# Performance work log

Hardware: AMD Instinct MI355X
Metric: run time of the kernel (lower is better)

## Reference

```python
import jax, jax.numpy as jnp
import numpy as np

B, D, UD = 32, 1024, 256          # batch, chunks_dim, units_dim
ENT, NENT = 32, 64                # entity_size, n_entities
S, C = NENT * ENT, NENT + 1       # src_len (units), n_chunks
NEG_INF = float('-inf')


def setup_inputs() -> dict:
    key = jax.random.key(0)
    ks = jax.random.split(key, 9)
    source = jax.random.normal(ks[0], (B, D), jnp.float32)
    high_level_repr = jax.random.normal(ks[1], (C, B, D), jnp.float32)
    pos_embs = jax.random.normal(ks[2], (S, B, UD), jnp.float32)
    low_level_repr = jax.random.normal(ks[3], (S, B, D), jnp.float32)
    low_level_mask = jax.random.randint(ks[4], (NENT, B, ENT), 0, 2).astype(bool)
    high_level_mask = jax.random.randint(ks[5], (1, B, C), 0, 2).astype(bool)
    high_level_mask = high_level_mask.at[..., 0].set(False)  # avoid all-masked chunk softmax
    W_unit = jax.random.normal(ks[6], (UD, D), jnp.float32) / np.sqrt(D)
    W_chunk = jax.random.normal(ks[7], (D, D), jnp.float32) / np.sqrt(D)
    W_out = jax.random.normal(ks[8], (D, 2 * D), jnp.float32) / np.sqrt(2 * D)
    return {"source": source, "high_level_repr": high_level_repr, "pos_embs": pos_embs,
            "low_level_repr": low_level_repr, "low_level_mask": low_level_mask,
            "high_level_mask": high_level_mask, "W_unit": W_unit, "W_chunk": W_chunk,
            "W_out": W_out}


def reference(source, high_level_repr, pos_embs, low_level_repr,
              low_level_mask, high_level_mask, W_unit, W_chunk, W_out):
    # batch-first views (torch transposes(0,1))
    hl = jnp.swapaxes(high_level_repr, 0, 1)    # (B, C, D)
    ll = jnp.swapaxes(low_level_repr, 0, 1)     # (B, S, D)
    pe = jnp.swapaxes(pos_embs, 0, 1)           # (B, S, UD)
    ll_mask = jnp.swapaxes(low_level_mask, 0, 1)   # (B, NENT, ENT)
    hl_mask = jnp.swapaxes(high_level_mask, 0, 1)  # (B, 1, C)

    # 'general' attention scorers, tgt_len == 1
    q_u = source @ W_unit.T                      # (B, UD)
    align_units = jnp.einsum('bd,bsd->bs', q_u, pe)        # (B, S)
    q_c = source @ W_chunk.T                     # (B, D)
    align_chunks = jnp.einsum('bd,bcd->bc', q_c, hl)[:, None, :]  # (B, 1, C)

    # low-level masked softmax per entity, NaN rows -> 0
    au = align_units.reshape(B, NENT, ENT)
    au = jnp.where(ll_mask, NEG_INF, au)
    au = jax.nn.softmax(au, axis=-1)
    all_masked = jnp.all(ll_mask, axis=-1)       # (B, NENT) rows that were NaN
    au = jnp.where(all_masked[..., None], 0.0, au)
    au = au.reshape(B, 1, S)

    # high-level masked softmax, drop chunk 0, inflate to unit granularity
    ac = jnp.where(hl_mask, NEG_INF, align_chunks)
    ac = jax.nn.softmax(ac, axis=-1)[:, :, 1:]   # (B, 1, C-1)
    ac_inflated = jnp.repeat(ac, ENT, axis=-1)   # (B, 1, S)

    align_vectors = ac_inflated * au             # (B, 1, S)
    c = jnp.einsum('bts,bsd->btd', align_vectors, ll)  # (B, 1, D)
    concat = jnp.concatenate([c, source[:, None, :]], axis=-1).reshape(B, 2 * D)
    attn_h = jnp.tanh(concat @ W_out.T)          # (B, D); tanh since attn_type='general'

    return (attn_h,
            align_vectors[:, 0, :],              # (B, S)
            ac[:, 0, :],                         # (B, C-1)
            au.reshape(B, S))                    # (B, S)
```

## Files before the change

kernel.cpp:

```cpp
#include <hip/hip_runtime.h>

#define B 32
#define D 1024
#define UD 256
#define ENT 32
#define NENT 64
#define S 2048
#define C 65

__device__ __forceinline__ float dot4(float4 w, const float* q) {
    return w.x * q[0] + w.y * q[1] + w.z * q[2] + w.w * q[3];
}

__global__ __launch_bounds__(256) void k_proj(const float* __restrict__ src,
                                              const float* __restrict__ Wu,
                                              const float* __restrict__ Wc,
                                              float* __restrict__ qu,
                                              float* __restrict__ qc) {
    __shared__ alignas(16) float s_src[4][D];
    __shared__ float red[4][64][4];
    int t = threadIdx.x, rg = blockIdx.x, bg = blockIdx.y;
    for (int f = t; f < 4 * (D / 4); f += 256) {
        int bb = f >> 8, i4 = f & 255;
        float4 v = *(const float4*)(src + (size_t)(bg * 4 + bb) * D + i4 * 4);
        *(float4*)(&s_src[bb][i4 * 4]) = v;
    }
    __syncthreads();
    int jl = t & 63, kq = t >> 6;
    int gj = rg * 64 + jl;
    const float* wrow = (gj < UD) ? (Wu + (size_t)gj * D) : (Wc + (size_t)(gj - UD) * D);
    const float4* wp = (const float4*)wrow + kq * 64;
    float acc[4] = {0.f, 0.f, 0.f, 0.f};
#pragma unroll 4
    for (int i = 0; i < 64; ++i) {
        float4 w = wp[i];
        int k = kq * 256 + i * 4;
#pragma unroll
        for (int bb = 0; bb < 4; ++bb) acc[bb] += dot4(w, &s_src[bb][k]);
    }
#pragma unroll
    for (int bb = 0; bb < 4; ++bb) red[kq][jl][bb] = acc[bb];
    __syncthreads();
    {
        int jl2 = t & 63, bb = t >> 6;
        float s = red[0][jl2][bb] + red[1][jl2][bb] + red[2][jl2][bb] + red[3][jl2][bb];
        int gj2 = rg * 64 + jl2, b = bg * 4 + bb;
        if (gj2 < UD) qu[b * UD + gj2] = s;
        else qc[b * D + (gj2 - UD)] = s;
    }
}

__global__ __launch_bounds__(256) void k_units(const float* __restrict__ pe,
                                               const int* __restrict__ lmask,
                                               const float* __restrict__ qu,
                                               float* __restrict__ out_au) {
    __shared__ alignas(16) float q[UD];
    __shared__ float part[256];
    int n = blockIdx.x, b = blockIdx.y, t = threadIdx.x;
    q[t] = qu[b * UD + t];
    __syncthreads();
    int e = t >> 3, r = t & 7;
    const float4* pp = (const float4*)(pe + (size_t)(n * ENT + e) * B * UD + (size_t)b * UD) + r * 8;
    float acc = 0.f;
#pragma unroll
    for (int i = 0; i < 8; ++i) acc += dot4(pp[i], &q[(r * 8 + i) * 4]);
    part[t] = acc;
    __syncthreads();
    if (t < ENT) {
        float sc = 0.f;
#pragma unroll
        for (int r2 = 0; r2 < 8; ++r2) sc += part[t * 8 + r2];
        bool m = lmask[(size_t)n * B * ENT + b * ENT + t] != 0;
        float v = m ? -1e30f : sc;
        float mx = v;
        for (int o = 16; o >= 1; o >>= 1) mx = fmaxf(mx, __shfl_xor(mx, o));
        float p = m ? 0.f : __expf(v - mx);
        float sm = p;
        for (int o = 16; o >= 1; o >>= 1) sm += __shfl_xor(sm, o);
        out_au[b * S + n * ENT + t] = (sm > 0.f) ? (p / sm) : 0.f;
    }
}

__global__ __launch_bounds__(256) void k_chunks(const float* __restrict__ hl,
                                                const int* __restrict__ hmask,
                                                const float* __restrict__ qc,
                                                float* __restrict__ out_ac) {
    __shared__ alignas(16) float q[D];
    __shared__ float sc[C];
    __shared__ float red[2];
    int b = blockIdx.x, t = threadIdx.x;
    for (int i = t; i < D / 4; i += 256)
        *(float4*)(&q[i * 4]) = *(const float4*)(qc + (size_t)b * D + i * 4);
    __syncthreads();
    int w = t >> 6, l = t & 63;
    for (int c = w; c < C; c += 4) {
        const float4* hp = (const float4*)(hl + (size_t)(c * B + b) * D);
        float acc = 0.f;
#pragma unroll
        for (int i = 0; i < 4; ++i) {
            int f = l + 64 * i;
            float4 h = hp[f];
            acc += dot4(h, &q[f * 4]);
        }
        for (int o = 32; o >= 1; o >>= 1) acc += __shfl_xor(acc, o);
        if (l == 0) sc[c] = acc;
    }
    __syncthreads();
    if (t == 0) {
        float mx = -1e30f;
        for (int c = 0; c < C; ++c) {
            float v = hmask[b * C + c] ? -1e30f : sc[c];
            mx = fmaxf(mx, v);
        }
        float sm = 0.f;
        for (int c = 0; c < C; ++c) {
            float v = hmask[b * C + c] ? -1e30f : sc[c];
            sm += __expf(v - mx);
        }
        red[0] = mx;
        red[1] = sm;
    }
    __syncthreads();
    if (t >= 1 && t < C) {
        bool m = hmask[b * C + t] != 0;
        float p = m ? 0.f : __expf(sc[t] - red[0]) / red[1];
        out_ac[b * NENT + (t - 1)] = p;
    }
}

__global__ __launch_bounds__(256) void k_ctx(const float* __restrict__ ll,
                                             const float* __restrict__ out_au,
                                             const float* __restrict__ out_ac,
                                             float* __restrict__ pf,
                                             float* __restrict__ out_av) {
    __shared__ float s_av[256];
    int ss = blockIdx.x, b = blockIdx.y, t = threadIdx.x;
    {
        int s = ss * 256 + t;
        int n = s >> 5;
        float a = out_ac[b * NENT + n] * out_au[b * S + s];
        s_av[t] = a;
        out_av[b * S + s] = a;
    }
    __syncthreads();
    float4 acc = {0.f, 0.f, 0.f, 0.f};
    const float4* base = (const float4*)(ll + (size_t)(ss * 256) * B * D + (size_t)b * D) + t;
#pragma unroll 8
    for (int j = 0; j < 256; ++j) {
        float4 x = base[(size_t)j * (B * D / 4)];
        float wv = s_av[j];
        acc.x += wv * x.x;
        acc.y += wv * x.y;
        acc.z += wv * x.z;
        acc.w += wv * x.w;
    }
    *(float4*)(pf + (size_t)ss * B * D + (size_t)b * D + t * 4) = acc;
}

__global__ __launch_bounds__(256) void k_red(const float* __restrict__ pf,
                                             float* __restrict__ cf) {
    int f = blockIdx.x * 256 + threadIdx.x;
    float s = 0.f;
#pragma unroll
    for (int ss = 0; ss < 8; ++ss) s += pf[(size_t)ss * B * D + f];
    cf[f] = s;
}

__global__ __launch_bounds__(256) void k_out(const float* __restrict__ Wo,
                                             const float* __restrict__ src,
                                             const float* __restrict__ cf,
                                             float* __restrict__ out_h) {
    __shared__ alignas(16) float cc[4][2 * D];
    __shared__ float red[4][64][4];
    int t = threadIdx.x, jg = blockIdx.x, bg = blockIdx.y;
    for (int f = t; f < 4 * (2 * D / 4); f += 256) {
        int bb = f >> 9, part = f & 511;
        int b = bg * 4 + bb;
        float4 v;
        if (part < 256) v = *(const float4*)(cf + (size_t)b * D + part * 4);
        else v = *(const float4*)(src + (size_t)b * D + (part - 256) * 4);
        *(float4*)(&cc[bb][part * 4]) = v;
    }
    __syncthreads();
    int jl = t & 63, kq = t >> 6;
    int j = jg * 64 + jl;
    const float4* wp = (const float4*)(Wo + (size_t)j * 2 * D) + kq * 128;
    float acc[4] = {0.f, 0.f, 0.f, 0.f};
#pragma unroll 4
    for (int i = 0; i < 128; ++i) {
        float4 w = wp[i];
        int k = kq * 512 + i * 4;
#pragma unroll
        for (int bb = 0; bb < 4; ++bb) acc[bb] += dot4(w, &cc[bb][k]);
    }
#pragma unroll
    for (int bb = 0; bb < 4; ++bb) red[kq][jl][bb] = acc[bb];
    __syncthreads();
    {
        int jl2 = t & 63, bb = t >> 6;
        float s = red[0][jl2][bb] + red[1][jl2][bb] + red[2][jl2][bb] + red[3][jl2][bb];
        out_h[(size_t)(bg * 4 + bb) * D + jg * 64 + jl2] = tanhf(s);
    }
}

extern "C" void kernel_launch(void* const* d_in, const int* in_sizes, int n_in,
                              void* d_out, int out_size, void* d_ws, size_t ws_size,
                              hipStream_t stream) {
    const float* src = (const float*)d_in[0];
    const float* hl = (const float*)d_in[1];
    const float* pe = (const float*)d_in[2];
    const float* ll = (const float*)d_in[3];
    const int* lmask = (const int*)d_in[4];
    const int* hmask = (const int*)d_in[5];
    const float* Wu = (const float*)d_in[6];
    const float* Wc = (const float*)d_in[7];
    const float* Wo = (const float*)d_in[8];

    float* out = (float*)d_out;
    float* out_h = out;
    float* out_av = out + B * D;
    float* out_ac = out_av + B * S;
    float* out_au = out_ac + B * NENT;

    float* ws = (float*)d_ws;
    float* qu = ws;
    float* qc = qu + B * UD;
    float* cf = qc + B * D;
    float* pf = cf + B * D;

    k_proj<<<dim3(20, 8), 256, 0, stream>>>(src, Wu, Wc, qu, qc);
    k_units<<<dim3(NENT, B), 256, 0, stream>>>(pe, lmask, qu, out_au);
    k_chunks<<<dim3(B), 256, 0, stream>>>(hl, hmask, qc, out_ac);
    k_ctx<<<dim3(8, B), 256, 0, stream>>>(ll, out_au, out_ac, pf, out_av);
    k_red<<<dim3(B * D / 256), 256, 0, stream>>>(pf, cf);
    k_out<<<dim3(16, 8), 256, 0, stream>>>(Wo, src, cf, out_h);
}
```

Measured before the change: 478.0 us.

## Coalesce GEMV weight reads, merge score kernels, split context into more slabs

The projection and output GEMVs now have each wavefront read one weight row with lane-contiguous float4 loads and reduce across the wave, replacing the per-thread strided row reads and the shared-memory reduction. The unit-score and chunk-score kernels become one launch, with a single extra block column per batch handling chunks. Unit scores are computed with coalesced row reads and wave reductions. The context kernel splits the source into 16 slabs instead of 8 to double the block count, which doubles the partial buffer that k_red must sum.

Result: no change. 479.1 us (+0.2%).

```diff
diff --git a/kernel.cpp b/kernel.cpp
--- a/kernel.cpp
+++ b/kernel.cpp
@@ -7,9 +7,17 @@
 #define NENT 64
 #define S 2048
 #define C 65
+#define NSLAB 16
+#define SROWS (S / NSLAB)
 
 __device__ __forceinline__ float dot4(float4 w, const float* q) {
     return w.x * q[0] + w.y * q[1] + w.z * q[2] + w.w * q[3];
+}
+
+__device__ __forceinline__ float wave_sum(float v) {
+#pragma unroll
+    for (int o = 32; o >= 1; o >>= 1) v += __shfl_xor(v, o);
+    return v;
 }
 
 __global__ __launch_bounds__(256) void k_proj(const float* __restrict__ src,
@@ -18,113 +26,115 @@
                                               float* __restrict__ qu,
                                               float* __restrict__ qc) {
     __shared__ alignas(16) float s_src[4][D];
-    __shared__ float red[4][64][4];
     int t = threadIdx.x, rg = blockIdx.x, bg = blockIdx.y;
     for (int f = t; f < 4 * (D / 4); f += 256) {
         int bb = f >> 8, i4 = f & 255;
-        float4 v = *(const float4*)(src + (size_t)(bg * 4 + bb) * D + i4 * 4);
-        *(float4*)(&s_src[bb][i4 * 4]) = v;
+        *(float4*)(&s_src[bb][i4 * 4]) =
+            *(const float4*)(src + (size_t)(bg * 4 + bb) * D + i4 * 4);
     }
     __syncthreads();
-    int jl = t & 63, kq = t >> 6;
-    int gj = rg * 64 + jl;
-    const float* wrow = (gj < UD) ? (Wu + (size_t)gj * D) : (Wc + (size_t)(gj - UD) * D);
-    const float4* wp = (const float4*)wrow + kq * 64;
-    float acc[4] = {0.f, 0.f, 0.f, 0.f};
-#pragma unroll 4
-    for (int i = 0; i < 64; ++i) {
-        float4 w = wp[i];
-        int k = kq * 256 + i * 4;
-#pragma unroll
-        for (int bb = 0; bb < 4; ++bb) acc[bb] += dot4(w, &s_src[bb][k]);
-    }
-#pragma unroll
-    for (int bb = 0; bb < 4; ++bb) red[kq][jl][bb] = acc[bb];
-    __syncthreads();
-    {
-        int jl2 = t & 63, bb = t >> 6;
-        float s = red[0][jl2][bb] + red[1][jl2][bb] + red[2][jl2][bb] + red[3][jl2][bb];
-        int gj2 = rg * 64 + jl2, b = bg * 4 + bb;
-        if (gj2 < UD) qu[b * UD + gj2] = s;
-        else qc[b * D + (gj2 - UD)] = s;
-    }
-}
-
-__global__ __launch_bounds__(256) void k_units(const float* __restrict__ pe,
-                                               const int* __restrict__ lmask,
-                                               const float* __restrict__ qu,
-                                               float* __restrict__ out_au) {
-    __shared__ alignas(16) float q[UD];
-    __shared__ float part[256];
-    int n = blockIdx.x, b = blockIdx.y, t = threadIdx.x;
-    q[t] = qu[b * UD + t];
-    __syncthreads();
-    int e = t >> 3, r = t & 7;
-    const float4* pp = (const float4*)(pe + (size_t)(n * ENT + e) * B * UD + (size_t)b * UD) + r * 8;
-    float acc = 0.f;
-#pragma unroll
-    for (int i = 0; i < 8; ++i) acc += dot4(pp[i], &q[(r * 8 + i) * 4]);
-    part[t] = acc;
-    __syncthreads();
-    if (t < ENT) {
-        float sc = 0.f;
-#pragma unroll
-        for (int r2 = 0; r2 < 8; ++r2) sc += part[t * 8 + r2];
-        bool m = lmask[(size_t)n * B * ENT + b * ENT + t] != 0;
-        float v = m ? -1e30f : sc;
-        float mx = v;
-        for (int o = 16; o >= 1; o >>= 1) mx = fmaxf(mx, __shfl_xor(mx, o));
-        float p = m ? 0.f : __expf(v - mx);
-        float sm = p;
-        for (int o = 16; o >= 1; o >>= 1) sm += __shfl_xor(sm, o);
-        out_au[b * S + n * ENT + t] = (sm > 0.f) ? (p / sm) : 0.f;
-    }
-}
-
-__global__ __launch_bounds__(256) void k_chunks(const float* __restrict__ hl,
+    int w = t >> 6, l = t & 63;
+#pragma unroll
+    for (int pass = 0; pass < 8; ++pass) {
+        int r = pass * 4 + w;
+        int gj = rg * 32 + r;
+        const float4* wrow = (const float4*)((gj < UD) ? (Wu + (size_t)gj * D)
+                                                       : (Wc + (size_t)(gj - UD) * D));
+        float acc[4] = {0.f, 0.f, 0.f, 0.f};
+#pragma unroll
+        for (int p = 0; p < 4; ++p) {
+            float4 wv = wrow[p * 64 + l];
+            int k = p * 256 + l * 4;
+#pragma unroll
+            for (int bb = 0; bb < 4; ++bb) acc[bb] += dot4(wv, &s_src[bb][k]);
+        }
+#pragma unroll
+        for (int bb = 0; bb < 4; ++bb) acc[bb] = wave_sum(acc[bb]);
+        if (l == 0) {
+#pragma unroll
+            for (int bb = 0; bb < 4; ++bb) {
+                int b = bg * 4 + bb;
+                if (gj < UD) qu[b * UD + gj] = acc[bb];
+                else qc[b * D + (gj - UD)] = acc[bb];
+            }
+        }
+    }
+}
+
+__global__ __launch_bounds__(256) void k_scores(const float* __restrict__ pe,
+                                                const float* __restrict__ hl,
+                                                const int* __restrict__ lmask,
                                                 const int* __restrict__ hmask,
+                                                const float* __restrict__ qu,
                                                 const float* __restrict__ qc,
+                                                float* __restrict__ out_au,
                                                 float* __restrict__ out_ac) {
     __shared__ alignas(16) float q[D];
     __shared__ float sc[C];
-    __shared__ float red[2];
-    int b = blockIdx.x, t = threadIdx.x;
-    for (int i = t; i < D / 4; i += 256)
-        *(float4*)(&q[i * 4]) = *(const float4*)(qc + (size_t)b * D + i * 4);
-    __syncthreads();
-    int w = t >> 6, l = t & 63;
-    for (int c = w; c < C; c += 4) {
-        const float4* hp = (const float4*)(hl + (size_t)(c * B + b) * D);
-        float acc = 0.f;
-#pragma unroll
-        for (int i = 0; i < 4; ++i) {
-            int f = l + 64 * i;
-            float4 h = hp[f];
-            acc += dot4(h, &q[f * 4]);
-        }
-        for (int o = 32; o >= 1; o >>= 1) acc += __shfl_xor(acc, o);
-        if (l == 0) sc[c] = acc;
-    }
-    __syncthreads();
-    if (t == 0) {
-        float mx = -1e30f;
-        for (int c = 0; c < C; ++c) {
-            float v = hmask[b * C + c] ? -1e30f : sc[c];
-            mx = fmaxf(mx, v);
-        }
-        float sm = 0.f;
-        for (int c = 0; c < C; ++c) {
-            float v = hmask[b * C + c] ? -1e30f : sc[c];
-            sm += __expf(v - mx);
-        }
-        red[0] = mx;
-        red[1] = sm;
-    }
-    __syncthreads();
-    if (t >= 1 && t < C) {
-        bool m = hmask[b * C + t] != 0;
-        float p = m ? 0.f : __expf(sc[t] - red[0]) / red[1];
-        out_ac[b * NENT + (t - 1)] = p;
+    __shared__ float red2[2];
+    int x = blockIdx.x, b = blockIdx.y, t = threadIdx.x;
+    if (x < NENT) {
+        int n = x;
+        if (t < UD) q[t] = qu[b * UD + t];
+        __syncthreads();
+        int w = t >> 6, l = t & 63;
+#pragma unroll
+        for (int pass = 0; pass < 8; ++pass) {
+            int e = pass * 4 + w;
+            const float4* row = (const float4*)pe + (size_t)((n * ENT + e) * B + b) * (UD / 4);
+            float acc = wave_sum(dot4(row[l], &q[l * 4]));
+            if (l == 0) sc[e] = acc;
+        }
+        __syncthreads();
+        if (t < ENT) {
+            bool m = lmask[(size_t)n * B * ENT + b * ENT + t] != 0;
+            float v = m ? -1e30f : sc[t];
+            float mx = v;
+#pragma unroll
+            for (int o = 16; o >= 1; o >>= 1) mx = fmaxf(mx, __shfl_xor(mx, o));
+            float p = m ? 0.f : __expf(v - mx);
+            float sm = p;
+#pragma unroll
+            for (int o = 16; o >= 1; o >>= 1) sm += __shfl_xor(sm, o);
+            out_au[b * S + n * ENT + t] = (sm > 0.f) ? (p / sm) : 0.f;
+        }
+    } else {
+        for (int i = t; i < D / 4; i += 256)
+            *(float4*)(&q[i * 4]) = *(const float4*)(qc + (size_t)b * D + i * 4);
+        __syncthreads();
+        int w = t >> 6, l = t & 63;
+        for (int c = w; c < C; c += 4) {
+            const float4* hp = (const float4*)(hl + (size_t)(c * B + b) * D);
+            float acc = 0.f;
+#pragma unroll
+            for (int i = 0; i < 4; ++i) {
+                int f = l + 64 * i;
+                acc += dot4(hp[f], &q[f * 4]);
+            }
+            acc = wave_sum(acc);
+            if (l == 0) sc[c] = acc;
+        }
+        __syncthreads();
+        if (t == 0) {
+            float mx = -1e30f;
+            for (int c = 0; c < C; ++c) {
+                float v = hmask[b * C + c] ? -1e30f : sc[c];
+                mx = fmaxf(mx, v);
+            }
+            float sm = 0.f;
+            for (int c = 0; c < C; ++c) {
+                float v = hmask[b * C + c] ? -1e30f : sc[c];
+                sm += __expf(v - mx);
+            }
+            red2[0] = mx;
+            red2[1] = sm;
+        }
+        __syncthreads();
+        if (t >= 1 && t < C) {
+            bool m = hmask[b * C + t] != 0;
+            float p = m ? 0.f : __expf(sc[t] - red2[0]) / red2[1];
+            out_ac[b * NENT + (t - 1)] = p;
+        }
     }
 }
 
@@ -133,10 +143,10 @@
                                              const float* __restrict__ out_ac,
                                              float* __restrict__ pf,
                                              float* __restrict__ out_av) {
-    __shared__ float s_av[256];
+    __shared__ float s_av[SROWS];
     int ss = blockIdx.x, b = blockIdx.y, t = threadIdx.x;
-    {
-        int s = ss * 256 + t;
+    if (t < SROWS) {
+        int s = ss * SROWS + t;
         int n = s >> 5;
         float a = out_ac[b * NENT + n] * out_au[b * S + s];
         s_av[t] = a;
@@ -144,9 +154,9 @@
     }
     __syncthreads();
     float4 acc = {0.f, 0.f, 0.f, 0.f};
-    const float4* base = (const float4*)(ll + (size_t)(ss * 256) * B * D + (size_t)b * D) + t;
+    const float4* base = (const float4*)ll + ((size_t)(ss * SROWS) * B + b) * (D / 4) + t;
 #pragma unroll 8
-    for (int j = 0; j < 256; ++j) {
+    for (int j = 0; j < SROWS; ++j) {
         float4 x = base[(size_t)j * (B * D / 4)];
         float wv = s_av[j];
         acc.x += wv * x.x;
@@ -154,7 +164,7 @@
         acc.z += wv * x.z;
         acc.w += wv * x.w;
     }
-    *(float4*)(pf + (size_t)ss * B * D + (size_t)b * D + t * 4) = acc;
+    *(float4*)(pf + (size_t)(ss * B + b) * D + t * 4) = acc;
 }
 
 __global__ __launch_bounds__(256) void k_red(const float* __restrict__ pf,
@@ -162,7 +172,7 @@
     int f = blockIdx.x * 256 + threadIdx.x;
     float s = 0.f;
 #pragma unroll
-    for (int ss = 0; ss < 8; ++ss) s += pf[(size_t)ss * B * D + f];
+    for (int ss = 0; ss < NSLAB; ++ss) s += pf[(size_t)ss * B * D + f];
     cf[f] = s;
 }
 
@@ -171,7 +181,6 @@
                                              const float* __restrict__ cf,
                                              float* __restrict__ out_h) {
     __shared__ alignas(16) float cc[4][2 * D];
-    __shared__ float red[4][64][4];
     int t = threadIdx.x, jg = blockIdx.x, bg = blockIdx.y;
     for (int f = t; f < 4 * (2 * D / 4); f += 256) {
         int bb = f >> 9, part = f & 511;
@@ -182,24 +191,27 @@
         *(float4*)(&cc[bb][part * 4]) = v;
     }
     __syncthreads();
-    int jl = t & 63, kq = t >> 6;
-    int j = jg * 64 + jl;
-    const float4* wp = (const float4*)(Wo + (size_t)j * 2 * D) + kq * 128;
-    float acc[4] = {0.f, 0.f, 0.f, 0.f};
-#pragma unroll 4
-    for (int i = 0; i < 128; ++i) {
-        float4 w = wp[i];
-        int k = kq * 512 + i * 4;
-#pragma unroll
-        for (int bb = 0; bb < 4; ++bb) acc[bb] += dot4(w, &cc[bb][k]);
-    }
-#pragma unroll
-    for (int bb = 0; bb < 4; ++bb) red[kq][jl][bb] = acc[bb];
-    __syncthreads();
-    {
-        int jl2 = t & 63, bb = t >> 6;
-        float s = red[0][jl2][bb] + red[1][jl2][bb] + red[2][jl2][bb] + red[3][jl2][bb];
-        out_h[(size_t)(bg * 4 + bb) * D + jg * 64 + jl2] = tanhf(s);
+    int w = t >> 6, l = t & 63;
+#pragma unroll
+    for (int pass = 0; pass < 16; ++pass) {
+        int r = pass * 4 + w;
+        int j = jg * 64 + r;
+        const float4* wrow = (const float4*)(Wo + (size_t)j * 2 * D);
+        float acc[4] = {0.f, 0.f, 0.f, 0.f};
+#pragma unroll
+        for (int p = 0; p < 8; ++p) {
+            float4 wv = wrow[p * 64 + l];
+            int k = p * 256 + l * 4;
+#pragma unroll
+            for (int bb = 0; bb < 4; ++bb) acc[bb] += dot4(wv, &cc[bb][k]);
+        }
+#pragma unroll
+        for (int bb = 0; bb < 4; ++bb) acc[bb] = wave_sum(acc[bb]);
+        if (l == 0) {
+#pragma unroll
+            for (int bb = 0; bb < 4; ++bb)
+                out_h[(size_t)(bg * 4 + bb) * D + j] = tanhf(acc[bb]);
+        }
     }
 }
 
@@ -228,10 +240,10 @@
     float* cf = qc + B * D;
     float* pf = cf + B * D;
 
-    k_proj<<<dim3(20, 8), 256, 0, stream>>>(src, Wu, Wc, qu, qc);
-    k_units<<<dim3(NENT, B), 256, 0, stream>>>(pe, lmask, qu, out_au);
-    k_chunks<<<dim3(B), 256, 0, stream>>>(hl, hmask, qc, out_ac);
-    k_ctx<<<dim3(8, B), 256, 0, stream>>>(ll, out_au, out_ac, pf, out_av);
+    k_proj<<<dim3(40, 8), 256, 0, stream>>>(src, Wu, Wc, qu, qc);
+    k_scores<<<dim3(NENT + 1, B), 256, 0, stream>>>(pe, hl, lmask, hmask, qu, qc,
+                                                    out_au, out_ac);
+    k_ctx<<<dim3(NSLAB, B), 256, 0, stream>>>(ll, out_au, out_ac, pf, out_av);
     k_red<<<dim3(B * D / 256), 256, 0, stream>>>(pf, cf);
     k_out<<<dim3(16, 8), 256, 0, stream>>>(Wo, src, cf, out_h);
 }
```
